# Kernel optimization log

Measured on AMD Instinct MI355X. Metric: run time of the kernel, lower is better.

Reference implementation:

```python
import jax, jax.numpy as jnp
import numpy as np
from jax import lax

DIM = 64
HEADS = 4
B, Q, V = 8, 128, 128


def _modrelu(z, b):
    m = jnp.abs(z)
    return z * (jax.nn.relu(m + b) / (m + 1e-5))


def _eunn_unitary(h, th1, ph1, th2, ph2, om):
    # tunable-style EUNN, capacity 2: even-pair rotations, odd-pair rotations, diagonal phase
    d = h.shape[-1]
    # layer 1: pairs (0,1),(2,3),...
    hp = h.reshape(*h.shape[:-1], d // 2, 2)
    a, b = hp[..., 0], hp[..., 1]
    c1, s1, e1 = jnp.cos(th1), jnp.sin(th1), jnp.exp(1j * ph1)
    h = jnp.stack([e1 * (c1 * a - s1 * b), s1 * a + c1 * b], -1).reshape(h.shape)
    # layer 2: pairs (1,2),(3,4),...,(d-3,d-2); endpoints pass through
    mid = h[..., 1:d - 1].reshape(*h.shape[:-1], d // 2 - 1, 2)
    a, b = mid[..., 0], mid[..., 1]
    c2, s2, e2 = jnp.cos(th2), jnp.sin(th2), jnp.exp(1j * ph2)
    mid2 = jnp.stack([e2 * (c2 * a - s2 * b), s2 * a + c2 * b], -1).reshape(*h.shape[:-1], d - 2)
    h = jnp.concatenate([h[..., :1], mid2, h[..., d - 1:]], -1)
    return h * jnp.exp(1j * om)


def _forward(queries, values, U_re, U_im, bias, theta1, phi1, theta2, phi2, omega, W_dense, b_dense):
    Bq, Qq, d = queries.shape
    Vv = values.shape[1]
    # quadratic (query, value) expansion -> [B*Q, V, 2d]
    dq = jnp.broadcast_to(queries[:, :, None, :], (Bq, Qq, Vv, d))
    dv = jnp.broadcast_to(values[:, None, :, :], (Bq, Qq, Vv, d))
    x = jnp.concatenate([dq, dv], -1).reshape(Bq * Qq, Vv, 2 * d)
    U = (U_re + 1j * U_im)  # [H, 2d, d] complex input kernel per head
    Ux = jnp.einsum('nvi,hij->hvnj', x.astype(jnp.complex64), U)  # [H, V, N, d]

    def run_head(Ux_h, t1, p1, t2, p2, om, bh):
        def step(h, u):
            h2 = _modrelu(_eunn_unitary(h, t1, p1, t2, p2, om) + u, bh)
            return h2, None
        h0 = jnp.zeros(Ux_h.shape[1:], dtype=jnp.complex64)  # [N, d]
        hT, _ = lax.scan(step, h0, Ux_h)
        return hT  # final state, as Keras RNN with return_sequences=False

    outs = jax.vmap(run_head)(Ux, theta1, phi1, theta2, phi2, omega, bias)  # [H, N, d]
    acc = jnp.real(outs).transpose(1, 0, 2).reshape(Bq * Qq, HEADS * d)
    y = acc @ W_dense + b_dense
    return y.reshape(Bq, Qq, d)


def setup_inputs() -> dict:
    key = jax.random.key(0)
    ks = jax.random.split(key, 12)
    pi = np.pi
    return {
        'queries': jax.random.normal(ks[0], (B, Q, DIM), jnp.float32),
        'values': jax.random.normal(ks[1], (B, V, DIM), jnp.float32),
        'U_re': jax.random.normal(ks[2], (HEADS, 2 * DIM, DIM), jnp.float32) * (1.0 / np.sqrt(2 * DIM)),
        'U_im': jax.random.normal(ks[3], (HEADS, 2 * DIM, DIM), jnp.float32) * (1.0 / np.sqrt(2 * DIM)),
        'bias': jax.random.normal(ks[4], (HEADS, DIM), jnp.float32) * 0.01,
        'theta1': jax.random.uniform(ks[5], (HEADS, DIM // 2), jnp.float32, -pi, pi),
        'phi1': jax.random.uniform(ks[6], (HEADS, DIM // 2), jnp.float32, -pi, pi),
        'theta2': jax.random.uniform(ks[7], (HEADS, DIM // 2 - 1), jnp.float32, -pi, pi),
        'phi2': jax.random.uniform(ks[8], (HEADS, DIM // 2 - 1), jnp.float32, -pi, pi),
        'omega': jax.random.uniform(ks[9], (HEADS, DIM), jnp.float32, -pi, pi),
        'W_dense': jax.random.normal(ks[10], (HEADS * DIM, DIM), jnp.float32) * (1.0 / np.sqrt(HEADS * DIM)),
        'b_dense': jnp.zeros((DIM,), jnp.float32),
    }


def reference(queries, values, U_re, U_im, bias, theta1, phi1, theta2, phi2, omega, W_dense, b_dense):
    return _forward(queries, values, U_re, U_im, bias, theta1, phi1, theta2, phi2, omega, W_dense, b_dense)
```

## Files before the change

kernel.cpp:

```cpp
#include <hip/hip_runtime.h>
#include <math.h>

#define DIM 64
#define HEADS 4
#define BB 8
#define QQ 128
#define VV 128
#define NN (BB*QQ)

__device__ __forceinline__ float dpp_swap1(float x) {
    return __int_as_float(__builtin_amdgcn_update_dpp(
        0, __float_as_int(x), 0xB1 , 0xF, 0xF, true));
}

__global__ __launch_bounds__(256) void k_av(const float* __restrict__ values,
                                            const float* __restrict__ U_re,
                                            const float* __restrict__ U_im,
                                            float2* __restrict__ Av) {
    int tid = blockIdx.x * blockDim.x + threadIdx.x;
    int w = tid >> 6;
    int j = tid & 63;
    int h = w >> 10;
    int rem = w & 1023;
    float vself = values[rem * DIM + j];
    const float* ur = U_re + (h * 2 * DIM + DIM) * DIM + j;
    const float* ui = U_im + (h * 2 * DIM + DIM) * DIM + j;
    float ar = 0.f, ai = 0.f;
    #pragma unroll
    for (int i = 0; i < DIM; ++i) {
        float vi = __shfl(vself, i, 64);
        ar = fmaf(vi, ur[i * DIM], ar);
        ai = fmaf(vi, ui[i * DIM], ai);
    }
    Av[(h * 1024 + rem) * DIM + j] = make_float2(ar, ai);
}

__global__ __launch_bounds__(256) void k_rnn_dense(
        const float* __restrict__ queries,
        const float* __restrict__ U_re,
        const float* __restrict__ U_im,
        const float* __restrict__ bias,
        const float* __restrict__ theta1,
        const float* __restrict__ phi1,
        const float* __restrict__ theta2,
        const float* __restrict__ phi2,
        const float* __restrict__ omega,
        const float2* __restrict__ Av,
        const float* __restrict__ W_dense,
        const float* __restrict__ b_dense,
        float* __restrict__ y) {
    int n = blockIdx.x;
    int t = threadIdx.x;
    int h = t >> 6;
    int j = t & 63;
    int b = n >> 7;

    int k1 = j >> 1;
    float th1 = theta1[h * 32 + k1], ph1 = phi1[h * 32 + k1];
    float c1 = cosf(th1), s1 = sinf(th1);
    float A1r, A1i, B1r, B1i;
    if ((j & 1) == 0) {
        float er = cosf(ph1), ei = sinf(ph1);
        A1r = er * c1; A1i = ei * c1;
        B1r = -er * s1; B1i = -ei * s1;
    } else {
        A1r = c1; A1i = 0.f;
        B1r = s1; B1i = 0.f;
    }

    float A2r, A2i, B2r, B2i;
    int p2lane;
    if (j == 0 || j == 63) {
        A2r = 1.f; A2i = 0.f; B2r = 0.f; B2i = 0.f; p2lane = j;
    } else {
        int k2 = (j - 1) >> 1;
        float th2 = theta2[h * 31 + k2], ph2 = phi2[h * 31 + k2];
        float c2 = cosf(th2), s2 = sinf(th2);
        if (j & 1) {
            float er = cosf(ph2), ei = sinf(ph2);
            A2r = er * c2; A2i = ei * c2;
            B2r = -er * s2; B2i = -ei * s2;
            p2lane = j + 1;
        } else {
            A2r = c2; A2i = 0.f;
            B2r = s2; B2i = 0.f;
            p2lane = j - 1;
        }
    }
    {
        float om = omega[h * 64 + j];
        float eor = cosf(om), eoi = sinf(om);
        float tr, ti;
        tr = A2r * eor - A2i * eoi; ti = A2r * eoi + A2i * eor; A2r = tr; A2i = ti;
        tr = B2r * eor - B2i * eoi; ti = B2r * eoi + B2i * eor; B2r = tr; B2i = ti;
    }

    float bj = bias[h * 64 + j];

    float qself = queries[n * DIM + j];
    const float* ur = U_re + (h * 2 * DIM) * DIM + j;
    const float* ui = U_im + (h * 2 * DIM) * DIM + j;
    float uqr = 0.f, uqi = 0.f;
    #pragma unroll
    for (int i = 0; i < DIM; ++i) {
        float qi = __shfl(qself, i, 64);
        uqr = fmaf(qi, ur[i * DIM], uqr);
        uqi = fmaf(qi, ui[i * DIM], uqi);
    }

    const float2* Avp = Av + (h * 8 + b) * VV * DIM + j;

    float hr = 0.f, hi = 0.f;
    #pragma unroll 4
    for (int v = 0; v < VV; ++v) {
        float2 av = Avp[v * DIM];
        float pr = dpp_swap1(hr);
        float pi = dpp_swap1(hi);
        float t_r = A1r * hr - A1i * hi + B1r * pr - B1i * pi;
        float t_i = A1r * hi + A1i * hr + B1r * pi + B1i * pr;
        float qr  = __shfl(t_r, p2lane, 64);
        float qi2 = __shfl(t_i, p2lane, 64);
        float s_r = A2r * t_r - A2i * t_i + B2r * qr - B2i * qi2;
        float s_i = A2r * t_i + A2i * t_r + B2r * qi2 + B2i * qr;
        float zr = s_r + uqr + av.x;
        float zi = s_i + uqi + av.y;
        float q2 = fmaf(zr, zr, fmaf(zi, zi, 1e-30f));
        float rs = __builtin_amdgcn_rsqf(q2);
        float m = q2 * rs;
        float tpos = fmaxf(m + bj, 0.f);
        float inv = __builtin_amdgcn_rcpf(m + 1e-5f);
        float sc = tpos * inv;
        hr = zr * sc;
        hi = zi * sc;
    }

    __shared__ float s_acc[HEADS * DIM];
    __shared__ float s_part[256];
    s_acc[h * 64 + j] = hr;
    __syncthreads();

    int qq = t >> 6;
    int jj = t & 63;
    const float* Wp = W_dense + (qq * 64) * DIM + jj;
    float part = 0.f;
    #pragma unroll 8
    for (int k = 0; k < 64; ++k)
        part = fmaf(s_acc[qq * 64 + k], Wp[k * DIM], part);
    s_part[t] = part;
    __syncthreads();
    if (t < 64) {
        float s = b_dense[jj] + s_part[jj] + s_part[64 + jj]
                + s_part[128 + jj] + s_part[192 + jj];
        y[n * DIM + jj] = s;
    }
}

extern "C" void kernel_launch(void* const* d_in, const int* in_sizes, int n_in,
                              void* d_out, int out_size, void* d_ws, size_t ws_size,
                              hipStream_t stream) {
    const float* queries = (const float*)d_in[0];
    const float* values  = (const float*)d_in[1];
    const float* U_re    = (const float*)d_in[2];
    const float* U_im    = (const float*)d_in[3];
    const float* bias    = (const float*)d_in[4];
    const float* theta1  = (const float*)d_in[5];
    const float* phi1    = (const float*)d_in[6];
    const float* theta2  = (const float*)d_in[7];
    const float* phi2    = (const float*)d_in[8];
    const float* omega   = (const float*)d_in[9];
    const float* W_dense = (const float*)d_in[10];
    const float* b_dense = (const float*)d_in[11];
    float* y = (float*)d_out;

    float2* Av = (float2*)d_ws;

    k_av<<<1024, 256, 0, stream>>>(values, U_re, U_im, Av);
    k_rnn_dense<<<1024, 256, 0, stream>>>(queries, U_re, U_im, bias, theta1,
                                          phi1, theta2, phi2, omega, Av,
                                          W_dense, b_dense, y);
}
```

Baseline: 126.4 us.

## Process two query rows per block and replace shuffles with wave-shift DPP

Each block of the RNN kernel now runs two independent query sequences (q and q+64), which share the Av loads and the rotation coefficients. The two recurrences interleave to hide latency, and the grid is halved. The second-layer neighbour exchange now uses wave-shift-left and wave-shift-right DPP instead of ds_bpermute shuffles, at the cost of extra multiplies with zeroed coefficients. Query and value rows are read as scalar-uniform loads instead of lane shuffles. The risks are that halving the grid to 512 blocks lowers occupancy, and that wave_shl/wave_shr DPP controls may not be supported on gfx9.5 (CDNA wave shifts are legacy), which could make the results wrong.

After: 133.6 us. 5.7% more time.

```diff
diff --git a/kernel.cpp b/kernel.cpp
--- a/kernel.cpp
+++ b/kernel.cpp
@@ -10,7 +10,15 @@
 
 __device__ __forceinline__ float dpp_swap1(float x) {
     return __int_as_float(__builtin_amdgcn_update_dpp(
-        0, __float_as_int(x), 0xB1 , 0xF, 0xF, true));
+        0, __float_as_int(x), 0xB1, 0xF, 0xF, true));
+}
+__device__ __forceinline__ float dpp_wshr1(float x) {
+    return __int_as_float(__builtin_amdgcn_update_dpp(
+        0, __float_as_int(x), 0x138, 0xF, 0xF, true));
+}
+__device__ __forceinline__ float dpp_wshl1(float x) {
+    return __int_as_float(__builtin_amdgcn_update_dpp(
+        0, __float_as_int(x), 0x130, 0xF, 0xF, true));
 }
 
 __global__ __launch_bounds__(256) void k_av(const float* __restrict__ values,
@@ -20,15 +28,15 @@
     int tid = blockIdx.x * blockDim.x + threadIdx.x;
     int w = tid >> 6;
     int j = tid & 63;
-    int h = w >> 10;
-    int rem = w & 1023;
-    float vself = values[rem * DIM + j];
+    int h = __builtin_amdgcn_readfirstlane(w >> 10);
+    int rem = __builtin_amdgcn_readfirstlane(w & 1023);
+    const float* vrow = values + rem * DIM;
     const float* ur = U_re + (h * 2 * DIM + DIM) * DIM + j;
     const float* ui = U_im + (h * 2 * DIM + DIM) * DIM + j;
     float ar = 0.f, ai = 0.f;
-    #pragma unroll
+    #pragma unroll 16
     for (int i = 0; i < DIM; ++i) {
-        float vi = __shfl(vself, i, 64);
+        float vi = vrow[i];
         ar = fmaf(vi, ur[i * DIM], ar);
         ai = fmaf(vi, ui[i * DIM], ai);
     }
@@ -49,11 +57,13 @@
         const float* __restrict__ W_dense,
         const float* __restrict__ b_dense,
         float* __restrict__ y) {
-    int n = blockIdx.x;
+    int b = blockIdx.x >> 6;
+    int q = blockIdx.x & 63;
     int t = threadIdx.x;
     int h = t >> 6;
     int j = t & 63;
-    int b = n >> 7;
+    int n0 = b * 128 + q;
+    int n1 = n0 + 64;
 
     int k1 = j >> 1;
     float th1 = theta1[h * 32 + k1], ph1 = phi1[h * 32 + k1];
@@ -68,10 +78,9 @@
         B1r = s1; B1i = 0.f;
     }
 
-    float A2r, A2i, B2r, B2i;
-    int p2lane;
+    float A2r, A2i, BLr, BLi, BRr, BRi;
     if (j == 0 || j == 63) {
-        A2r = 1.f; A2i = 0.f; B2r = 0.f; B2i = 0.f; p2lane = j;
+        A2r = 1.f; A2i = 0.f; BLr = 0.f; BLi = 0.f; BRr = 0.f; BRi = 0.f;
     } else {
         int k2 = (j - 1) >> 1;
         float th2 = theta2[h * 31 + k2], ph2 = phi2[h * 31 + k2];
@@ -79,12 +88,12 @@
         if (j & 1) {
             float er = cosf(ph2), ei = sinf(ph2);
             A2r = er * c2; A2i = ei * c2;
-            B2r = -er * s2; B2i = -ei * s2;
-            p2lane = j + 1;
+            BLr = -er * s2; BLi = -ei * s2;
+            BRr = 0.f; BRi = 0.f;
         } else {
             A2r = c2; A2i = 0.f;
-            B2r = s2; B2i = 0.f;
-            p2lane = j - 1;
+            BRr = s2; BRi = 0.f;
+            BLr = 0.f; BLi = 0.f;
         }
     }
     {
@@ -92,66 +101,86 @@
         float eor = cosf(om), eoi = sinf(om);
         float tr, ti;
         tr = A2r * eor - A2i * eoi; ti = A2r * eoi + A2i * eor; A2r = tr; A2i = ti;
-        tr = B2r * eor - B2i * eoi; ti = B2r * eoi + B2i * eor; B2r = tr; B2i = ti;
-    }
-
+        tr = BLr * eor - BLi * eoi; ti = BLr * eoi + BLi * eor; BLr = tr; BLi = ti;
+        tr = BRr * eor - BRi * eoi; ti = BRr * eoi + BRi * eor; BRr = tr; BRi = ti;
+    }
     float bj = bias[h * 64 + j];
 
-    float qself = queries[n * DIM + j];
+    const float* qrow0 = queries + n0 * DIM;
+    const float* qrow1 = queries + n1 * DIM;
     const float* ur = U_re + (h * 2 * DIM) * DIM + j;
     const float* ui = U_im + (h * 2 * DIM) * DIM + j;
-    float uqr = 0.f, uqi = 0.f;
-    #pragma unroll
+    float uq0r = 0.f, uq0i = 0.f, uq1r = 0.f, uq1i = 0.f;
+    #pragma unroll 16
     for (int i = 0; i < DIM; ++i) {
-        float qi = __shfl(qself, i, 64);
-        uqr = fmaf(qi, ur[i * DIM], uqr);
-        uqi = fmaf(qi, ui[i * DIM], uqi);
-    }
-
-    const float2* Avp = Av + (h * 8 + b) * VV * DIM + j;
-
-    float hr = 0.f, hi = 0.f;
+        float a0 = qrow0[i];
+        float a1 = qrow1[i];
+        float wr = ur[i * DIM], wi = ui[i * DIM];
+        uq0r = fmaf(a0, wr, uq0r); uq0i = fmaf(a0, wi, uq0i);
+        uq1r = fmaf(a1, wr, uq1r); uq1i = fmaf(a1, wi, uq1i);
+    }
+
+    const float2* Avp = Av + (h * 1024 + b * 128) * DIM + j;
+
+    float h0r = 0.f, h0i = 0.f, h1r = 0.f, h1i = 0.f;
     #pragma unroll 4
     for (int v = 0; v < VV; ++v) {
         float2 av = Avp[v * DIM];
-        float pr = dpp_swap1(hr);
-        float pi = dpp_swap1(hi);
-        float t_r = A1r * hr - A1i * hi + B1r * pr - B1i * pi;
-        float t_i = A1r * hi + A1i * hr + B1r * pi + B1i * pr;
-        float qr  = __shfl(t_r, p2lane, 64);
-        float qi2 = __shfl(t_i, p2lane, 64);
-        float s_r = A2r * t_r - A2i * t_i + B2r * qr - B2i * qi2;
-        float s_i = A2r * t_i + A2i * t_r + B2r * qi2 + B2i * qr;
-        float zr = s_r + uqr + av.x;
-        float zi = s_i + uqi + av.y;
-        float q2 = fmaf(zr, zr, fmaf(zi, zi, 1e-30f));
-        float rs = __builtin_amdgcn_rsqf(q2);
-        float m = q2 * rs;
-        float tpos = fmaxf(m + bj, 0.f);
-        float inv = __builtin_amdgcn_rcpf(m + 1e-5f);
-        float sc = tpos * inv;
-        hr = zr * sc;
-        hi = zi * sc;
-    }
-
-    __shared__ float s_acc[HEADS * DIM];
+        {
+            float pr = dpp_swap1(h0r), pi = dpp_swap1(h0i);
+            float t_r = A1r * h0r - A1i * h0i + B1r * pr - B1i * pi;
+            float t_i = A1r * h0i + A1i * h0r + B1r * pi + B1i * pr;
+            float Lr = dpp_wshl1(t_r), Li = dpp_wshl1(t_i);
+            float Rr = dpp_wshr1(t_r), Ri = dpp_wshr1(t_i);
+            float s_r = A2r * t_r - A2i * t_i + BLr * Lr - BLi * Li + BRr * Rr - BRi * Ri;
+            float s_i = A2r * t_i + A2i * t_r + BLr * Li + BLi * Lr + BRr * Ri + BRi * Rr;
+            float zr = s_r + uq0r + av.x;
+            float zi = s_i + uq0i + av.y;
+            float q2 = fmaf(zr, zr, fmaf(zi, zi, 1e-30f));
+            float rs = __builtin_amdgcn_rsqf(q2);
+            float m = q2 * rs;
+            float sc = fmaxf(m + bj, 0.f) * __builtin_amdgcn_rcpf(m + 1e-5f);
+            h0r = zr * sc; h0i = zi * sc;
+        }
+        {
+            float pr = dpp_swap1(h1r), pi = dpp_swap1(h1i);
+            float t_r = A1r * h1r - A1i * h1i + B1r * pr - B1i * pi;
+            float t_i = A1r * h1i + A1i * h1r + B1r * pi + B1i * pr;
+            float Lr = dpp_wshl1(t_r), Li = dpp_wshl1(t_i);
+            float Rr = dpp_wshr1(t_r), Ri = dpp_wshr1(t_i);
+            float s_r = A2r * t_r - A2i * t_i + BLr * Lr - BLi * Li + BRr * Rr - BRi * Ri;
+            float s_i = A2r * t_i + A2i * t_r + BLr * Li + BLi * Lr + BRr * Ri + BRi * Rr;
+            float zr = s_r + uq1r + av.x;
+            float zi = s_i + uq1i + av.y;
+            float q2 = fmaf(zr, zr, fmaf(zi, zi, 1e-30f));
+            float rs = __builtin_amdgcn_rsqf(q2);
+            float m = q2 * rs;
+            float sc = fmaxf(m + bj, 0.f) * __builtin_amdgcn_rcpf(m + 1e-5f);
+            h1r = zr * sc; h1i = zi * sc;
+        }
+    }
+
+    __shared__ float s_acc[2][HEADS * DIM];
     __shared__ float s_part[256];
-    s_acc[h * 64 + j] = hr;
+    s_acc[0][h * 64 + j] = h0r;
+    s_acc[1][h * 64 + j] = h1r;
     __syncthreads();
 
-    int qq = t >> 6;
-    int jj = t & 63;
-    const float* Wp = W_dense + (qq * 64) * DIM + jj;
-    float part = 0.f;
-    #pragma unroll 8
-    for (int k = 0; k < 64; ++k)
-        part = fmaf(s_acc[qq * 64 + k], Wp[k * DIM], part);
-    s_part[t] = part;
+    {
+        int r = t >> 7, hf = (t >> 6) & 1, jj = t & 63;
+        const float* Wp = W_dense + (hf * 128) * DIM + jj;
+        const float* ap = &s_acc[r][hf * 128];
+        float part = 0.f;
+        #pragma unroll 8
+        for (int k = 0; k < 128; ++k)
+            part = fmaf(ap[k], Wp[k * DIM], part);
+        s_part[t] = part;
+    }
     __syncthreads();
-    if (t < 64) {
-        float s = b_dense[jj] + s_part[jj] + s_part[64 + jj]
-                + s_part[128 + jj] + s_part[192 + jj];
-        y[n * DIM + jj] = s;
+    if (t < 128) {
+        int r = t >> 6, jj = t & 63;
+        y[(n0 + r * 64) * DIM + jj] =
+            b_dense[jj] + s_part[r * 128 + jj] + s_part[r * 128 + 64 + jj];
     }
 }
 
@@ -175,7 +204,7 @@
     float2* Av = (float2*)d_ws;
 
     k_av<<<1024, 256, 0, stream>>>(values, U_re, U_im, Av);
-    k_rnn_dense<<<1024, 256, 0, stream>>>(queries, U_re, U_im, bias, theta1,
-                                          phi1, theta2, phi2, omega, Av,
-                                          W_dense, b_dense, y);
-}
+    k_rnn_dense<<<512, 256, 0, stream>>>(queries, U_re, U_im, bias, theta1,
+                                         phi1, theta2, phi2, omega, Av,
+                                         W_dense, b_dense, y);
+}
```
